# Optimization experiments

Measured on AMD Instinct MI355X. Metric: run time of the kernel, lower is better.

The kernel has to match this reference:

```python
import jax, jax.numpy as jnp
import numpy as np

B, T, I, H = 32768, 512, 2, 16  # batch, seq_len, input_size, hidden_size


def setup_inputs() -> dict:
    key = jax.random.key(0)
    ks = jax.random.split(key, 9)
    sc_i = 1.0 / np.sqrt(H)  # torch LSTM/Linear init scale ~ U(-1/sqrt(H), 1/sqrt(H)); use normal*scale
    return {
        "x": jax.random.normal(ks[0], (B, T, I), jnp.float32),
        "W_ih": jax.random.normal(ks[1], (4 * H, I), jnp.float32) * sc_i,
        "W_hh": jax.random.normal(ks[2], (4 * H, H), jnp.float32) * sc_i,
        "b_ih": jax.random.normal(ks[3], (4 * H,), jnp.float32) * sc_i,
        "b_hh": jax.random.normal(ks[4], (4 * H,), jnp.float32) * sc_i,
        "W1": jax.random.normal(ks[5], (H, H), jnp.float32) * sc_i,
        "b1": jax.random.normal(ks[6], (H,), jnp.float32) * sc_i,
        "W2": jax.random.normal(ks[7], (I, H), jnp.float32) * sc_i,
        "b2": jax.random.normal(ks[8], (I,), jnp.float32) * sc_i,
    }


def reference(x, W_ih, W_hh, b_ih, b_hh, W1, b1, W2, b2):
    # x: [B, T, I]. torch forward permutes to (T, B, I) and runs seq-first LSTM.
    # Precompute input projections for all timesteps (one big GEMM): [B, T, 4H]
    x_proj = jnp.einsum('bti,gi->btg', x, W_ih) + b_ih + b_hh
    Whh_T = W_hh.T  # [H, 4H]

    def step(carry, xt):
        h, c = carry                      # [B, H] each
        gates = xt + h @ Whh_T            # [B, 4H]
        i, f, g, o = jnp.split(gates, 4, axis=-1)  # torch gate order: i, f, g, o
        i = jax.nn.sigmoid(i)
        f = jax.nn.sigmoid(f)
        g = jnp.tanh(g)
        o = jax.nn.sigmoid(o)
        c = f * c + i * g
        h = o * jnp.tanh(c)
        return (h, c), None

    bsz = x.shape[0]
    h0 = jnp.zeros((bsz, W_hh.shape[1]), x.dtype)
    c0 = jnp.zeros_like(h0)
    (h_last, _), _ = jax.lax.scan(step, (h0, c0), jnp.swapaxes(x_proj, 0, 1))
    # MLP head on last hidden state: Linear -> tanh -> Linear
    y = jnp.tanh(h_last @ W1.T + b1) @ W2.T + b2  # [B, I]
    return y
```

## Files before the change

kernel.cpp:

```cpp
#include <hip/hip_runtime.h>


#define T_STEPS 512
#define LOG2E 1.44269504088896340736f

typedef __bf16 bf16x8 __attribute__((ext_vector_type(8)));
typedef float  f32x4  __attribute__((ext_vector_type(4)));
typedef float  f32x2  __attribute__((ext_vector_type(2)));
typedef unsigned int u32x4 __attribute__((ext_vector_type(4)));

union frag_u { u32x4 u; bf16x8 v; };

#if __has_builtin(__builtin_amdgcn_exp2f)
__device__ __forceinline__ float fexp2(float x) { return __builtin_amdgcn_exp2f(x); }
#else
__device__ __forceinline__ float fexp2(float x) { return exp2f(x); }
#endif
#if __has_builtin(__builtin_amdgcn_rcpf)
__device__ __forceinline__ float frcp(float x) { return __builtin_amdgcn_rcpf(x); }
#else
__device__ __forceinline__ float frcp(float x) { return 1.0f / x; }
#endif

__device__ __forceinline__ unsigned dup_hi(float h) {
    unsigned hb = __float_as_uint(h);
#if __has_builtin(__builtin_amdgcn_perm)
    return __builtin_amdgcn_perm(hb, hb, 0x03020302u);
#else
    return (hb >> 16) | (hb & 0xFFFF0000u);
#endif
}
__device__ __forceinline__ unsigned lo_with_x(float res, unsigned xq) {
#if __has_builtin(__builtin_amdgcn_perm)
    return __builtin_amdgcn_perm(xq, __float_as_uint(res), 0x07060302u);
#else
    return (__float_as_uint(res) >> 16) | (xq & 0xFFFF0000u);
#endif
}
__device__ __forceinline__ unsigned pack_hilo(float h) {
    unsigned hb = __float_as_uint(h);
    float    res = h - __uint_as_float(hb & 0xFFFF0000u);
#if __has_builtin(__builtin_amdgcn_perm)
    return __builtin_amdgcn_perm(__float_as_uint(res), hb, 0x07060302u);
#else
    return (hb >> 16) | (__float_as_uint(res) & 0xFFFF0000u);
#endif
}
__device__ __forceinline__ unsigned bfhi(float v) {
    return __float_as_uint(v) & 0xFFFF0000u;
}
__device__ __forceinline__ unsigned make_xq(float nx0, float nx1, int q) {
    const float xs = (q & 2) ? nx1 : nx0;
    const unsigned h16 = bfhi(xs);
    const unsigned l16 = bfhi(xs - __uint_as_float(h16));
    return (q & 1) ? l16 : h16;
}

__device__ __forceinline__ void lstm_step(
    const frag_u& BhI, const frag_u& BlI,
    frag_u& BhO, frag_u& BlO,
    float cs[4],
    const frag_u A1[4], const frag_u A2[4], const f32x4 biasf[4],
    unsigned xqn)
{
    f32x4 acc[4];
    #pragma unroll
    for (int t = 0; t < 4; ++t)
        acc[t] = __builtin_amdgcn_mfma_f32_16x16x32_bf16(A1[t].v, BhI.v, biasf[t], 0, 0, 0);

    #pragma unroll
    for (int t = 0; t < 4; ++t) {
        acc[t] = __builtin_amdgcn_mfma_f32_16x16x32_bf16(A2[t].v, BlI.v, acc[t], 0, 0, 0);

        f32x2 eIF, eGO;
        eIF.x = fexp2(acc[t][0]);
        eIF.y = fexp2(acc[t][1]);
        eGO.x = fexp2(acc[t][2]);
        eGO.y = fexp2(acc[t][3]);
        const f32x2 pA = eIF + 1.0f;
        const f32x2 pB = eGO + 1.0f;
        const f32x2 PP = pA * pB;
        const float R  = frcp(PP.x * PP.y);
        const float Gm = fmaf(2.0f * LOG2E, eGO.x, -2.0f * LOG2E);
        const float u1 = fmaf(PP.x * pB.y, cs[t], Gm * PP.y);
        const float csn = u1 * R;
        cs[t] = csn;
        const float C2 = fexp2(csn);
        const float tc = fmaf(-2.0f, frcp(C2 + 1.0f), 1.0f);
        const float hn = (PP.x * pA.y) * R * tc;

        const unsigned hb = __float_as_uint(hn);
        BhO.u[t] = dup_hi(hn);
        const float resf = hn - __uint_as_float(hb & 0xFFFF0000u);
        BlO.u[t] = lo_with_x(resf, xqn);
    }
}

__global__ __launch_bounds__(256, 2)
void lstm_mfma_kernel(const float* __restrict__ x,
                      const float* __restrict__ W_ih,
                      const float* __restrict__ W_hh,
                      const float* __restrict__ b_ih,
                      const float* __restrict__ b_hh,
                      const float* __restrict__ W1,
                      const float* __restrict__ b1,
                      const float* __restrict__ W2,
                      const float* __restrict__ b2,
                      float* __restrict__ out)
{
    __shared__ float hsm[4][16][16];

    const int tid  = threadIdx.x;
    const int wv   = tid >> 6;
    const int lane = tid & 63;
    const int e    = lane & 15;
    const int q    = lane >> 4;
    const int m    = lane & 15;

    const float gsc[4] = { -LOG2E, -LOG2E, 2.0f * LOG2E, -LOG2E };

    frag_u A1[4], A2[4];
    f32x4  biasf[4];
    #pragma unroll
    for (int t = 0; t < 4; ++t) {
        const int   g  = m & 3;
        const int   Rr = g * 16 + 4 * t + (m >> 2);
        const float sc = gsc[g];

        const float xw0 = W_ih[Rr * 2 + 0] * sc;
        const float xw1 = W_ih[Rr * 2 + 1] * sc;
        const unsigned x0h = bfhi(xw0);
        const unsigned x0l = bfhi(xw0 - __uint_as_float(x0h));
        const unsigned x1h = bfhi(xw1);
        const unsigned x1l = bfhi(xw1 - __uint_as_float(x1h));
        const unsigned cw0 = (q < 2) ? x0h : x1h;
        const unsigned cw1 = (q < 2) ? x0l : x1l;

        #pragma unroll
        for (int w = 0; w < 4; ++w) {
            const float whh = W_hh[Rr * 16 + 4 * w + q] * sc;
            A1[t].u[w] = pack_hilo(whh);
            A2[t].u[w] = __float_as_uint(whh) >> 16;
        }
        A2[t].u[0] |= cw0;
        A2[t].u[1] |= cw1;

        #pragma unroll
        for (int j = 0; j < 4; ++j) {
            const int Rb = j * 16 + 4 * t + q;
            biasf[t][j] = (b_ih[Rb] + b_hh[Rb]) * gsc[j];
        }
    }

    const int gelem = blockIdx.x * 64 + wv * 16 + e;
    const float4* xp = (const float4*)(x + (size_t)gelem * (T_STEPS * 2));

    frag_u BhA, BlA, BhB, BlB;
    float  cs[4] = {0.f, 0.f, 0.f, 0.f};

    float4 xv = xp[0];

    {
        const unsigned xq0 = make_xq(xv.x, xv.y, q);
        #pragma unroll
        for (int w = 0; w < 4; ++w) { BhA.u[w] = 0u; BlA.u[w] = xq0; }
    }

    for (int t2 = 0; t2 < T_STEPS / 2; ++t2) {
        const float4 xnext = xp[(t2 + 1) & (T_STEPS / 2 - 1)];

        const unsigned xq1 = make_xq(xv.z, xv.w, q);
        const unsigned xq2 = make_xq(xnext.x, xnext.y, q);

        lstm_step(BhA, BlA, BhB, BlB, cs, A1, A2, biasf, xq1);
        lstm_step(BhB, BlB, BhA, BlA, cs, A1, A2, biasf, xq2);

        xv = xnext;
    }

    #pragma unroll
    for (int r = 0; r < 4; ++r) {
        const float hval = __uint_as_float(BhA.u[r] << 16) +
                           __uint_as_float(BlA.u[r] << 16);
        hsm[wv][e][4 * r + q] = hval;
    }

    float hv[16];
    #pragma unroll
    for (int j = 0; j < 4; ++j) {
        const float4 t4 = *(const float4*)&hsm[wv][e][4 * j];
        hv[4 * j + 0] = t4.x; hv[4 * j + 1] = t4.y;
        hv[4 * j + 2] = t4.z; hv[4 * j + 3] = t4.w;
    }

    float z[4];
    #pragma unroll
    for (int r = 0; r < 4; ++r) {
        const int mm = 4 * q + r;
        float a = b1[mm];
        #pragma unroll
        for (int j = 0; j < 16; ++j) a = fmaf(W1[mm * 16 + j], hv[j], a);
        const float E = fexp2(a * (2.0f * LOG2E));
        z[r] = fmaf(-2.0f, frcp(1.0f + E), 1.0f);
    }
    #pragma unroll
    for (int r = 0; r < 4; ++r) hsm[wv][e][4 * q + r] = z[r];

    if (q < 2) {
        float a = b2[q];
        #pragma unroll
        for (int j = 0; j < 16; ++j) a = fmaf(W2[q * 16 + j], hsm[wv][e][j], a);
        out[(size_t)gelem * 2 + q] = a;
    }
}

extern "C" void kernel_launch(void* const* d_in, const int* in_sizes, int n_in,
                              void* d_out, int out_size, void* d_ws, size_t ws_size,
                              hipStream_t stream) {
    const float* x    = (const float*)d_in[0];
    const float* W_ih = (const float*)d_in[1];
    const float* W_hh = (const float*)d_in[2];
    const float* b_ih = (const float*)d_in[3];
    const float* b_hh = (const float*)d_in[4];
    const float* W1   = (const float*)d_in[5];
    const float* b1   = (const float*)d_in[6];
    const float* W2   = (const float*)d_in[7];
    const float* b2   = (const float*)d_in[8];
    float* out = (float*)d_out;

    lstm_mfma_kernel<<<dim3(512), dim3(256), 0, stream>>>(
        x, W_ih, W_hh, b_ih, b_hh, W1, b1, W2, b2, out);
}
```

Baseline: 497.0 us.

## Replace exp-based gate activations with rational tanh approximations in LSTM step

Gate nonlinearities are rewritten from exp2-plus-reciprocal sigmoid and tanh into Padé-style rational polynomial approximations of tanh, with sigmoids expressed as half-scaled tanh. Weight and bias scaling are changed to match, and the hidden state is carried as 2h. Reciprocals are shared across gate pairs and cell pairs, trading transcendental instructions for more FMAs. The gate tanh path is not clamped, so accuracy at large pre-activations depends on how well the rational form holds there, and the cell tanh is clamped at ±12.

```diff
diff --git a/kernel.cpp b/kernel.cpp
--- a/kernel.cpp
+++ b/kernel.cpp
@@ -59,7 +59,7 @@
 __device__ __forceinline__ void lstm_step(
     const frag_u& BhI, const frag_u& BlI,
     frag_u& BhO, frag_u& BlO,
-    float cs[4],
+    float cst[4],
     const frag_u A1[4], const frag_u A2[4], const f32x4 biasf[4],
     unsigned xqn)
 {
@@ -69,30 +69,57 @@
         acc[t] = __builtin_amdgcn_mfma_f32_16x16x32_bf16(A1[t].v, BhI.v, biasf[t], 0, 0, 0);
 
     #pragma unroll
-    for (int t = 0; t < 4; ++t) {
-        acc[t] = __builtin_amdgcn_mfma_f32_16x16x32_bf16(A2[t].v, BlI.v, acc[t], 0, 0, 0);
-
-        f32x2 eIF, eGO;
-        eIF.x = fexp2(acc[t][0]);
-        eIF.y = fexp2(acc[t][1]);
-        eGO.x = fexp2(acc[t][2]);
-        eGO.y = fexp2(acc[t][3]);
-        const f32x2 pA = eIF + 1.0f;
-        const f32x2 pB = eGO + 1.0f;
-        const f32x2 PP = pA * pB;
-        const float R  = frcp(PP.x * PP.y);
-        const float Gm = fmaf(2.0f * LOG2E, eGO.x, -2.0f * LOG2E);
-        const float u1 = fmaf(PP.x * pB.y, cs[t], Gm * PP.y);
-        const float csn = u1 * R;
-        cs[t] = csn;
-        const float C2 = fexp2(csn);
-        const float tc = fmaf(-2.0f, frcp(C2 + 1.0f), 1.0f);
-        const float hn = (PP.x * pA.y) * R * tc;
-
-        const unsigned hb = __float_as_uint(hn);
-        BhO.u[t] = dup_hi(hn);
-        const float resf = hn - __uint_as_float(hb & 0xFFFF0000u);
-        BlO.u[t] = lo_with_x(resf, xqn);
+    for (int pp = 0; pp < 2; ++pp) {
+        float numc2[2], dc2[2], To2[2];
+        #pragma unroll
+        for (int tt = 0; tt < 2; ++tt) {
+            const int t = 2 * pp + tt;
+            acc[t] = __builtin_amdgcn_mfma_f32_16x16x32_bf16(A2[t].v, BlI.v, acc[t], 0, 0, 0);
+
+            f32x2 a, b;
+            a.x = acc[t][0]; a.y = acc[t][1];
+            b.x = acc[t][2]; b.y = acc[t][3];
+
+            const f32x2 ua = a * a, ub = b * b;
+            f32x2 na = ua * 21.0f + 1260.0f;  na = ua * na + 10395.0f;
+            f32x2 nb = ub * 21.0f + 1260.0f;  nb = ub * nb + 10395.0f;
+            const f32x2 numa = a * na;
+            const f32x2 numb = b * nb;
+            f32x2 da = ua + 210.0f; da = ua * da + 4725.0f; da = ua * da + 10395.0f;
+            f32x2 db = ub + 210.0f; db = ub * db + 4725.0f; db = ub * db + 10395.0f;
+
+            const float p1 = da.x * da.y, p2 = db.x * db.y;
+            const float r  = frcp(p1 * p2);
+            const float Ti = numa.x * ((da.y * p2) * r);
+            const float Tf = numa.y * ((da.x * p2) * r);
+            const float Tg = numb.x * ((db.y * p1) * r);
+            const float To = numb.y * ((db.x * p1) * r);
+
+            const float mf = fmaf(Tf, cst[t], cst[t]);
+            const float mg = fmaf(Ti, Tg, Tg);
+            const float sn = fmaf(0.5f, mf, mg);
+            cst[t] = sn;
+
+            const float yc = fminf(fmaxf(sn, -12.0f), 12.0f);
+            const float w  = yc * yc;
+            float nc = fmaf(w, 0.65625f, 157.5f);  nc = fmaf(w, nc, 5197.5f);
+            numc2[tt] = yc * nc;
+            float dc = fmaf(w, 0.015625f, 13.125f); dc = fmaf(w, dc, 1181.25f);
+            dc2[tt] = fmaf(w, dc, 10395.0f);
+            To2[tt] = To;
+        }
+        const float rq = frcp(dc2[0] * dc2[1]);
+        #pragma unroll
+        for (int tt = 0; tt < 2; ++tt) {
+            const int t = 2 * pp + tt;
+            const float Tc = numc2[tt] * (rq * dc2[1 - tt]);
+            const float h2 = fmaf(To2[tt], Tc, Tc);
+
+            const unsigned hb = __float_as_uint(h2);
+            BhO.u[t] = dup_hi(h2);
+            const float resf = h2 - __uint_as_float(hb & 0xFFFF0000u);
+            BlO.u[t] = lo_with_x(resf, xqn);
+        }
     }
 }
 
@@ -117,7 +144,8 @@
     const int q    = lane >> 4;
     const int m    = lane & 15;
 
-    const float gsc[4] = { -LOG2E, -LOG2E, 2.0f * LOG2E, -LOG2E };
+    const float gsc[4]  = { 0.5f, 0.5f, 1.0f, 0.5f };
+    const float gscW[4] = { 0.25f, 0.25f, 0.5f, 0.25f };
 
     frag_u A1[4], A2[4];
     f32x4  biasf[4];
@@ -125,7 +153,8 @@
     for (int t = 0; t < 4; ++t) {
         const int   g  = m & 3;
         const int   Rr = g * 16 + 4 * t + (m >> 2);
-        const float sc = gsc[g];
+        const float sc  = gsc[g];
+        const float scW = gscW[g];
 
         const float xw0 = W_ih[Rr * 2 + 0] * sc;
         const float xw1 = W_ih[Rr * 2 + 1] * sc;
@@ -138,7 +167,7 @@
 
         #pragma unroll
         for (int w = 0; w < 4; ++w) {
-            const float whh = W_hh[Rr * 16 + 4 * w + q] * sc;
+            const float whh = W_hh[Rr * 16 + 4 * w + q] * scW;
             A1[t].u[w] = pack_hilo(whh);
             A2[t].u[w] = __float_as_uint(whh) >> 16;
         }
@@ -156,7 +185,7 @@
     const float4* xp = (const float4*)(x + (size_t)gelem * (T_STEPS * 2));
 
     frag_u BhA, BlA, BhB, BlB;
-    float  cs[4] = {0.f, 0.f, 0.f, 0.f};
+    float  cst[4] = {0.f, 0.f, 0.f, 0.f};
 
     float4 xv = xp[0];
 
@@ -172,16 +201,16 @@
         const unsigned xq1 = make_xq(xv.z, xv.w, q);
         const unsigned xq2 = make_xq(xnext.x, xnext.y, q);
 
-        lstm_step(BhA, BlA, BhB, BlB, cs, A1, A2, biasf, xq1);
-        lstm_step(BhB, BlB, BhA, BlA, cs, A1, A2, biasf, xq2);
+        lstm_step(BhA, BlA, BhB, BlB, cst, A1, A2, biasf, xq1);
+        lstm_step(BhB, BlB, BhA, BlA, cst, A1, A2, biasf, xq2);
 
         xv = xnext;
     }
 
     #pragma unroll
     for (int r = 0; r < 4; ++r) {
-        const float hval = __uint_as_float(BhA.u[r] << 16) +
-                           __uint_as_float(BlA.u[r] << 16);
+        const float hval = 0.5f * (__uint_as_float(BhA.u[r] << 16) +
+                                   __uint_as_float(BlA.u[r] << 16));
         hsm[wv][e][4 * r + q] = hval;
     }
 
```

Result: slower. 617.4 us (+24.2%).

## Interleave two independent batch groups per wave to hide MFMA and transcendental latency

Applied to the files above, without the earlier changes.

Each wave now processes two independent 16-sequence groups at once. Their MFMAs and exp/rcp chains are interleaved stage by stage, so one group's dependent-latency bubbles are filled by the other's work. The grid is halved to 256 blocks and launch bounds drop to 1 block per CU, giving up occupancy-based latency hiding in exchange for instruction-level parallelism and roughly double the register use per thread. With 256 blocks on a 256-CU part, the machine gets exactly one block per CU.

```diff
diff --git a/kernel.cpp b/kernel.cpp
--- a/kernel.cpp
+++ b/kernel.cpp
@@ -56,47 +56,114 @@
     return (q & 1) ? l16 : h16;
 }
 
-__device__ __forceinline__ void lstm_step(
-    const frag_u& BhI, const frag_u& BlI,
-    frag_u& BhO, frag_u& BlO,
-    float cs[4],
+__device__ __forceinline__ void lstm_step_dual(
+    const frag_u BhI[2], const frag_u BlI[2],
+    frag_u BhO[2], frag_u BlO[2],
+    float cst[2][4],
     const frag_u A1[4], const frag_u A2[4], const f32x4 biasf[4],
-    unsigned xqn)
+    unsigned xqA, unsigned xqB)
 {
-    f32x4 acc[4];
-    #pragma unroll
-    for (int t = 0; t < 4; ++t)
-        acc[t] = __builtin_amdgcn_mfma_f32_16x16x32_bf16(A1[t].v, BhI.v, biasf[t], 0, 0, 0);
-
-    #pragma unroll
-    for (int t = 0; t < 4; ++t) {
-        acc[t] = __builtin_amdgcn_mfma_f32_16x16x32_bf16(A2[t].v, BlI.v, acc[t], 0, 0, 0);
-
-        f32x2 eIF, eGO;
-        eIF.x = fexp2(acc[t][0]);
-        eIF.y = fexp2(acc[t][1]);
-        eGO.x = fexp2(acc[t][2]);
-        eGO.y = fexp2(acc[t][3]);
-        const f32x2 pA = eIF + 1.0f;
-        const f32x2 pB = eGO + 1.0f;
-        const f32x2 PP = pA * pB;
-        const float R  = frcp(PP.x * PP.y);
-        const float Gm = fmaf(2.0f * LOG2E, eGO.x, -2.0f * LOG2E);
-        const float u1 = fmaf(PP.x * pB.y, cs[t], Gm * PP.y);
-        const float csn = u1 * R;
-        cs[t] = csn;
-        const float C2 = fexp2(csn);
-        const float tc = fmaf(-2.0f, frcp(C2 + 1.0f), 1.0f);
-        const float hn = (PP.x * pA.y) * R * tc;
-
-        const unsigned hb = __float_as_uint(hn);
-        BhO.u[t] = dup_hi(hn);
-        const float resf = hn - __uint_as_float(hb & 0xFFFF0000u);
-        BlO.u[t] = lo_with_x(resf, xqn);
-    }
-}
-
-__global__ __launch_bounds__(256, 2)
+    f32x4 acc[2][4];
+    #pragma unroll
+    for (int g = 0; g < 2; ++g)
+        #pragma unroll
+        for (int t = 0; t < 4; ++t)
+            acc[g][t] = __builtin_amdgcn_mfma_f32_16x16x32_bf16(A1[t].v, BhI[g].v, biasf[t], 0, 0, 0);
+    #pragma unroll
+    for (int g = 0; g < 2; ++g)
+        #pragma unroll
+        for (int t = 0; t < 4; ++t)
+            acc[g][t] = __builtin_amdgcn_mfma_f32_16x16x32_bf16(A2[t].v, BlI[g].v, acc[g][t], 0, 0, 0);
+
+    f32x2 eIF[2][4], eGO[2][4];
+    #pragma unroll
+    for (int g = 0; g < 2; ++g)
+        #pragma unroll
+        for (int t = 0; t < 4; ++t) {
+            eIF[g][t].x = fexp2(acc[g][t][0]);
+            eIF[g][t].y = fexp2(acc[g][t][1]);
+            eGO[g][t].x = fexp2(acc[g][t][2]);
+            eGO[g][t].y = fexp2(acc[g][t][3]);
+        }
+
+    float Gm[2][4];
+    #pragma unroll
+    for (int g = 0; g < 2; ++g)
+        #pragma unroll
+        for (int t = 0; t < 4; ++t)
+            Gm[g][t] = fmaf(2.0f * LOG2E, eGO[g][t].x, -2.0f * LOG2E);
+
+    f32x2 pA[2][4], pB[2][4];
+    #pragma unroll
+    for (int g = 0; g < 2; ++g)
+        #pragma unroll
+        for (int t = 0; t < 4; ++t) {
+            pA[g][t] = eIF[g][t] + 1.0f;
+            pB[g][t] = eGO[g][t] + 1.0f;
+        }
+
+    f32x2 PP[2][4];
+    #pragma unroll
+    for (int g = 0; g < 2; ++g)
+        #pragma unroll
+        for (int t = 0; t < 4; ++t)
+            PP[g][t] = pA[g][t] * pB[g][t];
+
+    float d[2][4], tso[2][4], tsf[2][4], gmp[2][4];
+    #pragma unroll
+    for (int g = 0; g < 2; ++g)
+        #pragma unroll
+        for (int t = 0; t < 4; ++t) {
+            d[g][t]   = PP[g][t].x * PP[g][t].y;
+            tso[g][t] = PP[g][t].x * pA[g][t].y;
+            tsf[g][t] = PP[g][t].x * pB[g][t].y;
+            gmp[g][t] = Gm[g][t]   * PP[g][t].y;
+        }
+
+    float R[2][4];
+    #pragma unroll
+    for (int g = 0; g < 2; ++g)
+        #pragma unroll
+        for (int t = 0; t < 4; ++t)
+            R[g][t] = frcp(d[g][t]);
+
+    float csn[2][4];
+    #pragma unroll
+    for (int g = 0; g < 2; ++g)
+        #pragma unroll
+        for (int t = 0; t < 4; ++t) {
+            csn[g][t] = fmaf(tsf[g][t], cst[g][t], gmp[g][t]) * R[g][t];
+            cst[g][t] = csn[g][t];
+        }
+
+    float C2[2][4];
+    #pragma unroll
+    for (int g = 0; g < 2; ++g)
+        #pragma unroll
+        for (int t = 0; t < 4; ++t)
+            C2[g][t] = fexp2(csn[g][t]);
+
+    float Rd[2][4];
+    #pragma unroll
+    for (int g = 0; g < 2; ++g)
+        #pragma unroll
+        for (int t = 0; t < 4; ++t)
+            Rd[g][t] = frcp(C2[g][t] + 1.0f);
+
+    #pragma unroll
+    for (int g = 0; g < 2; ++g)
+        #pragma unroll
+        for (int t = 0; t < 4; ++t) {
+            const float tc = fmaf(-2.0f, Rd[g][t], 1.0f);
+            const float hn = (tso[g][t] * R[g][t]) * tc;
+            const unsigned hb = __float_as_uint(hn);
+            BhO[g].u[t] = dup_hi(hn);
+            const float resf = hn - __uint_as_float(hb & 0xFFFF0000u);
+            BlO[g].u[t] = lo_with_x(resf, g ? xqB : xqA);
+        }
+}
+
+__global__ __launch_bounds__(256, 1)
 void lstm_mfma_kernel(const float* __restrict__ x,
                       const float* __restrict__ W_ih,
                       const float* __restrict__ W_hh,
@@ -108,7 +175,7 @@
                       const float* __restrict__ b2,
                       float* __restrict__ out)
 {
-    __shared__ float hsm[4][16][16];
+    __shared__ float hsm[2][4][16][16];
 
     const int tid  = threadIdx.x;
     const int wv   = tid >> 6;
@@ -152,65 +219,83 @@
         }
     }
 
-    const int gelem = blockIdx.x * 64 + wv * 16 + e;
-    const float4* xp = (const float4*)(x + (size_t)gelem * (T_STEPS * 2));
-
-    frag_u BhA, BlA, BhB, BlB;
-    float  cs[4] = {0.f, 0.f, 0.f, 0.f};
-
-    float4 xv = xp[0];
+    const int gelemA = blockIdx.x * 128 + wv * 32 + e;
+    const int gelemB = gelemA + 16;
+    const float4* xpA = (const float4*)(x + (size_t)gelemA * (T_STEPS * 2));
+    const float4* xpB = (const float4*)(x + (size_t)gelemB * (T_STEPS * 2));
+
+    frag_u BhP[2], BlP[2], BhQ[2], BlQ[2];
+    float  cst[2][4];
+    #pragma unroll
+    for (int g = 0; g < 2; ++g)
+        #pragma unroll
+        for (int t = 0; t < 4; ++t) cst[g][t] = 0.0f;
+
+    float4 xvA = xpA[0];
+    float4 xvB = xpB[0];
 
     {
-        const unsigned xq0 = make_xq(xv.x, xv.y, q);
-        #pragma unroll
-        for (int w = 0; w < 4; ++w) { BhA.u[w] = 0u; BlA.u[w] = xq0; }
+        const unsigned xA0 = make_xq(xvA.x, xvA.y, q);
+        const unsigned xB0 = make_xq(xvB.x, xvB.y, q);
+        #pragma unroll
+        for (int w = 0; w < 4; ++w) {
+            BhP[0].u[w] = 0u; BlP[0].u[w] = xA0;
+            BhP[1].u[w] = 0u; BlP[1].u[w] = xB0;
+        }
     }
 
     for (int t2 = 0; t2 < T_STEPS / 2; ++t2) {
-        const float4 xnext = xp[(t2 + 1) & (T_STEPS / 2 - 1)];
-
-        const unsigned xq1 = make_xq(xv.z, xv.w, q);
-        const unsigned xq2 = make_xq(xnext.x, xnext.y, q);
-
-        lstm_step(BhA, BlA, BhB, BlB, cs, A1, A2, biasf, xq1);
-        lstm_step(BhB, BlB, BhA, BlA, cs, A1, A2, biasf, xq2);
-
-        xv = xnext;
+        const float4 xnA = xpA[(t2 + 1) & (T_STEPS / 2 - 1)];
+        const float4 xnB = xpB[(t2 + 1) & (T_STEPS / 2 - 1)];
+
+        const unsigned xq1A = make_xq(xvA.z, xvA.w, q);
+        const unsigned xq1B = make_xq(xvB.z, xvB.w, q);
+        const unsigned xq2A = make_xq(xnA.x, xnA.y, q);
+        const unsigned xq2B = make_xq(xnB.x, xnB.y, q);
+
+        lstm_step_dual(BhP, BlP, BhQ, BlQ, cst, A1, A2, biasf, xq1A, xq1B);
+        lstm_step_dual(BhQ, BlQ, BhP, BlP, cst, A1, A2, biasf, xq2A, xq2B);
+
+        xvA = xnA; xvB = xnB;
     }
 
     #pragma unroll
-    for (int r = 0; r < 4; ++r) {
-        const float hval = __uint_as_float(BhA.u[r] << 16) +
-                           __uint_as_float(BlA.u[r] << 16);
-        hsm[wv][e][4 * r + q] = hval;
-    }
-
-    float hv[16];
-    #pragma unroll
-    for (int j = 0; j < 4; ++j) {
-        const float4 t4 = *(const float4*)&hsm[wv][e][4 * j];
-        hv[4 * j + 0] = t4.x; hv[4 * j + 1] = t4.y;
-        hv[4 * j + 2] = t4.z; hv[4 * j + 3] = t4.w;
-    }
-
-    float z[4];
-    #pragma unroll
-    for (int r = 0; r < 4; ++r) {
-        const int mm = 4 * q + r;
-        float a = b1[mm];
-        #pragma unroll
-        for (int j = 0; j < 16; ++j) a = fmaf(W1[mm * 16 + j], hv[j], a);
-        const float E = fexp2(a * (2.0f * LOG2E));
-        z[r] = fmaf(-2.0f, frcp(1.0f + E), 1.0f);
-    }
-    #pragma unroll
-    for (int r = 0; r < 4; ++r) hsm[wv][e][4 * q + r] = z[r];
-
-    if (q < 2) {
-        float a = b2[q];
-        #pragma unroll
-        for (int j = 0; j < 16; ++j) a = fmaf(W2[q * 16 + j], hsm[wv][e][j], a);
-        out[(size_t)gelem * 2 + q] = a;
+    for (int g = 0; g < 2; ++g) {
+        #pragma unroll
+        for (int r = 0; r < 4; ++r) {
+            const float hval = __uint_as_float(BhP[g].u[r] << 16) +
+                               __uint_as_float(BlP[g].u[r] << 16);
+            hsm[g][wv][e][4 * r + q] = hval;
+        }
+
+        float hv[16];
+        #pragma unroll
+        for (int j = 0; j < 4; ++j) {
+            const float4 t4 = *(const float4*)&hsm[g][wv][e][4 * j];
+            hv[4 * j + 0] = t4.x; hv[4 * j + 1] = t4.y;
+            hv[4 * j + 2] = t4.z; hv[4 * j + 3] = t4.w;
+        }
+
+        float z[4];
+        #pragma unroll
+        for (int r = 0; r < 4; ++r) {
+            const int mm = 4 * q + r;
+            float a = b1[mm];
+            #pragma unroll
+            for (int j = 0; j < 16; ++j) a = fmaf(W1[mm * 16 + j], hv[j], a);
+            const float E = fexp2(a * (2.0f * LOG2E));
+            z[r] = fmaf(-2.0f, frcp(1.0f + E), 1.0f);
+        }
+        #pragma unroll
+        for (int r = 0; r < 4; ++r) hsm[g][wv][e][4 * q + r] = z[r];
+
+        if (q < 2) {
+            float a = b2[q];
+            #pragma unroll
+            for (int j = 0; j < 16; ++j) a = fmaf(W2[q * 16 + j], hsm[g][wv][e][j], a);
+            const int gelem = g ? gelemB : gelemA;
+            out[(size_t)gelem * 2 + q] = a;
+        }
     }
 }
 
@@ -228,6 +313,6 @@
     const float* b2   = (const float*)d_in[8];
     float* out = (float*)d_out;
 
-    lstm_mfma_kernel<<<dim3(512), dim3(256), 0, stream>>>(
+    lstm_mfma_kernel<<<dim3(256), dim3(256), 0, stream>>>(
         x, W_ih, W_hh, b_ih, b_hh, W1, b1, W2, b2, out);
 }
```

Result: no change. 498.1 us (+0.2%).
